# Kernel optimization log

Measured on AMD Instinct MI355X. Metric: run time of the kernel, lower is better.

The kernel has to match this reference:

```python
import jax, jax.numpy as jnp
import numpy as np

INPUT_DIM = 128
NUM_CLASSES = 10
MAX_DEPTH = 8
HID = 16            # effective_transform_output_dim
TEMP = 1.0
EFF_IN = INPUT_DIM + 2          # root features + parent score + grandparent score
N_INTERNAL = 2 ** MAX_DEPTH - 1  # 255, level-order stacked
N_LEAVES = 2 ** MAX_DEPTH        # 256
BATCH = 32768


def setup_inputs() -> dict:
    key = jax.random.key(0)
    ks = jax.random.split(key, 6)
    x = jax.random.normal(ks[0], (BATCH, INPUT_DIM), jnp.float32)
    path_prob = jnp.ones((BATCH, 1), jnp.float32)
    W1 = jax.random.normal(ks[1], (N_INTERNAL, EFF_IN, HID), jnp.float32) * (1.0 / np.sqrt(EFF_IN))
    b1 = jax.random.normal(ks[2], (N_INTERNAL, HID), jnp.float32) * 0.01
    w2 = jax.random.normal(ks[3], (N_INTERNAL, HID), jnp.float32) * (1.0 / np.sqrt(HID))
    b2 = jax.random.normal(ks[4], (N_INTERNAL,), jnp.float32) * 0.01
    leaf_logits = jax.random.normal(ks[5], (N_LEAVES, NUM_CLASSES), jnp.float32)
    return {"x": x, "path_prob": path_prob, "W1": W1, "b1": b1,
            "w2": w2, "b2": b2, "leaf_logits": leaf_logits}


def reference(x, path_prob, W1, b1, w2, b2, leaf_logits):
    """Depth-batched soft binary tree: all 2^d nodes at depth d are processed
    as one batched GEMM instead of the original sequential recursion."""
    B = x.shape[0]
    pp = path_prob                              # [B, n_nodes_at_depth]
    parent = jnp.zeros((B, 1), x.dtype)         # parent decision scores (0 => unused at depth 0)
    grandp = jnp.zeros((B, 1), x.dtype)         # grandparent scores (0 => unused at depth 0,1)
    for d in range(MAX_DEPTH):
        lo, hi = 2 ** d - 1, 2 ** (d + 1) - 1   # level-order slice of this depth's nodes
        W1d = W1[lo:hi]                          # [N, EFF_IN, HID]
        # concat([x, parent, grandparent]) @ W1d without materializing the concat
        h = jnp.einsum('be,neh->bnh', x, W1d[:, :INPUT_DIM, :])
        h = h + parent[:, :, None] * W1d[None, :, INPUT_DIM, :]
        h = h + grandp[:, :, None] * W1d[None, :, INPUT_DIM + 1, :]
        t = jax.nn.relu(h + b1[lo:hi][None])                       # [B, N, HID]
        score = jnp.einsum('bnh,nh->bn', t, w2[lo:hi]) + b2[lo:hi][None]  # [B, N]
        p = jax.nn.sigmoid(score / TEMP)
        n = pp.shape[1]
        # children: left gets p, right gets 1-p; level-order interleave
        pp = jnp.stack([pp * p, pp * (1.0 - p)], axis=-1).reshape(B, 2 * n)
        grandp = jnp.repeat(parent, 2, axis=1)   # child's grandparent = node's parent
        parent = jnp.repeat(score, 2, axis=1)    # child's parent_out = this node's raw score
    # leaves: sum_n path_prob[:, n] * output_logits[n]
    return jnp.einsum('bn,nc->bc', pp, leaf_logits)
```

## Files before the change

kernel.cpp:

```cpp
#include <hip/hip_runtime.h>
#include <math.h>

namespace {

typedef __attribute__((ext_vector_type(8))) __fp16 f16x8;
typedef __attribute__((ext_vector_type(4))) float f32x4;

constexpr int IN_DIM = 128;
constexpr int EFF    = 130 * 16;
constexpr int NODES  = 255;
constexpr int TS     = 64;
constexpr int BLOCK  = 256;
constexpr int NC     = 10;

__global__ __launch_bounds__(256) void prep_w1(const float* __restrict__ W1,
                                               f16x8* __restrict__ wfrag) {
    __shared__ float xs[IN_DIM * 16];
    const int n = blockIdx.x, tid = threadIdx.x;
    const float4* src = (const float4*)(W1 + (size_t)n * EFF);
    ((float4*)xs)[tid]       = src[tid];
    ((float4*)xs)[tid + 256] = src[tid + 256];
    __syncthreads();
    const int l = tid & 63, t = tid >> 6;
    const int k0 = t * 32 + (l >> 4) * 8, hid = l & 15;
    f16x8 hv;
    #pragma unroll
    for (int j = 0; j < 8; ++j)
        hv[j] = (__fp16)xs[(k0 + j) * 16 + hid];
    wfrag[(n * 4 + t) * 64 + l] = hv;
}

__global__ __launch_bounds__(BLOCK) __attribute__((amdgpu_waves_per_eu(2, 2)))
void tree_mfma(
    const float* __restrict__ x, const float* __restrict__ path_prob,
    const float* __restrict__ W1, const float* __restrict__ b1,
    const float* __restrict__ w2, const float* __restrict__ b2,
    const float* __restrict__ leaf_logits,
    const f16x8* __restrict__ wfrag,
    float* __restrict__ out)
{
    __shared__ float pp[128][TS];
    __shared__ float scbuf[112][TS];

    const int tid  = threadIdx.x;
    const int wv   = tid >> 6, l = tid & 63;
    const int quad = l >> 4,   col = l & 15;
    const int s0   = blockIdx.x * TS;

    if (tid < TS) pp[0][tid] = path_prob[s0 + tid];

    f16x8 xh[4][4];
    #pragma unroll
    for (int t = 0; t < 4; ++t)
        #pragma unroll
        for (int mt = 0; mt < 4; ++mt) {
            const float* xp = x + (size_t)(s0 + mt * 16 + col) * IN_DIM + t * 32 + quad * 8;
            float4 v0 = ((const float4*)xp)[0];
            float4 v1 = ((const float4*)xp)[1];
            float vv[8] = {v0.x, v0.y, v0.z, v0.w, v1.x, v1.y, v1.z, v1.w};
            f16x8 hv;
            #pragma unroll
            for (int j = 0; j < 8; ++j) hv[j] = (__fp16)vv[j];
            xh[t][mt] = hv;
        }

    const int wbase[3] = {0, 64, 80};

    const int first_n = (wv == 0) ? 0 : (wv == 1) ? 2 : (wv == 2) ? 5 : 6;
    f16x8 wcur[4];
    #pragma unroll
    for (int t = 0; t < 4; ++t) wcur[t] = wfrag[(size_t)first_n * 256 + t * 64 + l];

    for (int d = 0; d < 7; ++d) {
        const int nd = 1 << d;
        float (*scW)[TS]  = (float(*)[TS])&scbuf[wbase[d % 3]][0];
        float (*scP)[TS]  = (float(*)[TS])&scbuf[wbase[(d + 2) % 3]][0];
        float (*scP2)[TS] = (float(*)[TS])&scbuf[wbase[(d + 1) % 3]][0];
        const int stride = 128 >> d, half = 64 >> d;

        for (int nl = wv; nl < nd; nl += 4) {
            const int n = nd - 1 + nl;
            const int nn = (nl + 4 < nd) ? (n + 4) : (2 * nd - 1 + wv);

            f16x8 wnext[4];
            {
                const f16x8* wnp = wfrag + (size_t)nn * 256 + l;
                #pragma unroll
                for (int t = 0; t < 4; ++t) wnext[t] = wnp[t * 64];
            }

            const float4 b1q = ((const float4*)(b1 + n * 16))[quad];
            const float4 w2q = ((const float4*)(w2 + n * 16))[quad];
            const float4 wpq = ((const float4*)(W1 + (size_t)n * EFF + 128 * 16))[quad];
            const float4 wgq = ((const float4*)(W1 + (size_t)n * EFF + 129 * 16))[quad];
            const float  b2v = b2[n];
            const int    slot = nl * stride;
            const float  ppar = pp[slot][l];
            float par[4], gp[4];
            #pragma unroll
            for (int mt = 0; mt < 4; ++mt) {
                const int scol = mt * 16 + col;
                par[mt] = (d >= 1) ? scP[nl >> 1][scol] : 0.0f;
                gp[mt]  = (d >= 2) ? scP2[nl >> 2][scol] : 0.0f;
            }

            f32x4 binit = {b1q.x, b1q.y, b1q.z, b1q.w};
            f32x4 acc[4] = {binit, binit, binit, binit};
            #pragma unroll
            for (int t = 0; t < 4; ++t) {
                #pragma unroll
                for (int mt = 0; mt < 4; ++mt)
                    acc[mt] = __builtin_amdgcn_mfma_f32_16x16x32_f16(wcur[t], xh[t][mt], acc[mt], 0, 0, 0);
            }

            float score01[4];
            #pragma unroll
            for (int mt = 0; mt < 4; ++mt) {
                const f32x4 a = acc[mt];
                const float pa = par[mt], ga = gp[mt];
                float ts = 0.0f;
                #pragma unroll
                for (int r = 0; r < 4; ++r) {
                    const float wpr = (r == 0) ? wpq.x : (r == 1) ? wpq.y : (r == 2) ? wpq.z : wpq.w;
                    const float wgr = (r == 0) ? wgq.x : (r == 1) ? wgq.y : (r == 2) ? wgq.z : wgq.w;
                    const float w2r = (r == 0) ? w2q.x : (r == 1) ? w2q.y : (r == 2) ? w2q.z : w2q.w;
                    const float h = fmaf(pa, wpr, fmaf(ga, wgr, a[r]));
                    ts = fmaf(fmaxf(h, 0.0f), w2r, ts);
                }
                ts += __shfl_xor(ts, 16);
                ts += __shfl_xor(ts, 32);
                score01[mt] = ts;
            }
            const float sa = (quad & 1) ? score01[1] : score01[0];
            const float sb = (quad & 1) ? score01[3] : score01[2];
            const float sv = ((quad & 2) ? sb : sa) + b2v;

            scW[nl][l] = sv;
            const float p = 1.0f / (1.0f + __expf(-sv));
            pp[slot][l]        = ppar * p;
            pp[slot + half][l] = ppar * (1.0f - p);

            #pragma unroll
            for (int t = 0; t < 4; ++t) wcur[t] = wnext[t];
        }
        __syncthreads();
    }

    float oacc[NC];
    #pragma unroll
    for (int c = 0; c < NC; ++c) oacc[c] = 0.0f;
    {
        float (*scP)[TS]  = (float(*)[TS])&scbuf[wbase[0]][0];
        float (*scP2)[TS] = (float(*)[TS])&scbuf[wbase[2]][0];

        for (int nl = wv; nl < 128; nl += 4) {
            const int n = 127 + nl;
            const int nn = (nl + 4 < 128) ? (n + 4) : 254;

            f16x8 wnext[4];
            {
                const f16x8* wnp = wfrag + (size_t)nn * 256 + l;
                #pragma unroll
                for (int t = 0; t < 4; ++t) wnext[t] = wnp[t * 64];
            }

            const float4 b1q = ((const float4*)(b1 + n * 16))[quad];
            const float4 w2q = ((const float4*)(w2 + n * 16))[quad];
            const float4 wpq = ((const float4*)(W1 + (size_t)n * EFF + 128 * 16))[quad];
            const float4 wgq = ((const float4*)(W1 + (size_t)n * EFF + 129 * 16))[quad];
            const float  b2v = b2[n];
            const float  ppar = pp[nl][l];
            float par[4], gp[4];
            #pragma unroll
            for (int mt = 0; mt < 4; ++mt) {
                const int scol = mt * 16 + col;
                par[mt] = scP[nl >> 1][scol];
                gp[mt]  = scP2[nl >> 2][scol];
            }

            f32x4 binit = {b1q.x, b1q.y, b1q.z, b1q.w};
            f32x4 acc[4] = {binit, binit, binit, binit};
            #pragma unroll
            for (int t = 0; t < 4; ++t) {
                #pragma unroll
                for (int mt = 0; mt < 4; ++mt)
                    acc[mt] = __builtin_amdgcn_mfma_f32_16x16x32_f16(wcur[t], xh[t][mt], acc[mt], 0, 0, 0);
            }

            float score01[4];
            #pragma unroll
            for (int mt = 0; mt < 4; ++mt) {
                const f32x4 a = acc[mt];
                const float pa = par[mt], ga = gp[mt];
                float ts = 0.0f;
                #pragma unroll
                for (int r = 0; r < 4; ++r) {
                    const float wpr = (r == 0) ? wpq.x : (r == 1) ? wpq.y : (r == 2) ? wpq.z : wpq.w;
                    const float wgr = (r == 0) ? wgq.x : (r == 1) ? wgq.y : (r == 2) ? wgq.z : wgq.w;
                    const float w2r = (r == 0) ? w2q.x : (r == 1) ? w2q.y : (r == 2) ? w2q.z : w2q.w;
                    const float h = fmaf(pa, wpr, fmaf(ga, wgr, a[r]));
                    ts = fmaf(fmaxf(h, 0.0f), w2r, ts);
                }
                ts += __shfl_xor(ts, 16);
                ts += __shfl_xor(ts, 32);
                score01[mt] = ts;
            }
            const float sa = (quad & 1) ? score01[1] : score01[0];
            const float sb = (quad & 1) ? score01[3] : score01[2];
            const float sv = ((quad & 2) ? sb : sa) + b2v;

            const float p = 1.0f / (1.0f + __expf(-sv));
            const float pL = ppar * p;
            const float pR = ppar * (1.0f - p);
            const float* llp = leaf_logits + (size_t)(2 * nl) * NC;
            #pragma unroll
            for (int c = 0; c < NC; ++c)
                oacc[c] = fmaf(pL, llp[c], fmaf(pR, llp[NC + c], oacc[c]));

            #pragma unroll
            for (int t = 0; t < 4; ++t) wcur[t] = wnext[t];
        }
    }

    __syncthreads();
    {
        float* red = &scbuf[0][0];
        #pragma unroll
        for (int c = 0; c < NC; ++c)
            red[(wv * 64 + l) * NC + c] = oacc[c];
    }
    __syncthreads();
    {
        const float* red = &scbuf[0][0];
        for (int i = tid; i < TS * NC; i += BLOCK) {
            float v = red[i] + red[640 + i] + red[1280 + i] + red[1920 + i];
            out[(size_t)s0 * NC + i] = v;
        }
    }
}

}

extern "C" void kernel_launch(void* const* d_in, const int* in_sizes, int n_in,
                              void* d_out, int out_size, void* d_ws, size_t ws_size,
                              hipStream_t stream) {
    const float* x           = (const float*)d_in[0];
    const float* path_prob   = (const float*)d_in[1];
    const float* W1          = (const float*)d_in[2];
    const float* b1          = (const float*)d_in[3];
    const float* w2          = (const float*)d_in[4];
    const float* b2          = (const float*)d_in[5];
    const float* leaf_logits = (const float*)d_in[6];
    float* out = (float*)d_out;

    const int batch = in_sizes[0] / IN_DIM;
    f16x8* wfrag = (f16x8*)d_ws;

    hipLaunchKernelGGL(prep_w1, dim3(NODES), dim3(256), 0, stream, W1, wfrag);
    hipLaunchKernelGGL(tree_mfma, dim3(batch / TS), dim3(BLOCK), 0, stream,
                       x, path_prob, W1, b1, w2, b2, leaf_logits, wfrag, out);
}
```

Before: 150.5 us.

## Software-pipeline node epilogue behind next node's weight load and MFMA

Replaces the register prefetch of the next node's weight fragments with a software pipeline. Each iteration loads its own weights, then runs the previous node's score epilogue (ReLU, w2 dot, sigmoid, pp/score stores) while that load is in flight, and only then issues its own MFMAs. The idea is to hide global load latency behind VALU work and to overlap the epilogue with MFMA execution. In exchange, the weight load is no longer a full iteration ahead, and more state (accumulators and per-node params) stays live, adding register pressure at two waves per EU.

```diff
diff --git a/kernel.cpp b/kernel.cpp
--- a/kernel.cpp
+++ b/kernel.cpp
@@ -30,6 +30,47 @@
     wfrag[(n * 4 + t) * 64 + l] = hv;
 }
 
+__device__ __forceinline__ void loadW(const f16x8* __restrict__ wfrag, int n, int l,
+                                      f16x8 (&w)[4]) {
+    const f16x8* wp = wfrag + (size_t)n * 256 + l;
+    #pragma unroll
+    for (int t = 0; t < 4; ++t) w[t] = wp[t * 64];
+}
+
+__device__ __forceinline__ void mfma16(const f16x8 (&w)[4], const f16x8 (&xh)[4][4],
+                                       f32x4 (&acc)[4]) {
+    #pragma unroll
+    for (int t = 0; t < 4; ++t)
+        #pragma unroll
+        for (int mt = 0; mt < 4; ++mt)
+            acc[mt] = __builtin_amdgcn_mfma_f32_16x16x32_f16(w[t], xh[t][mt], acc[mt], 0, 0, 0);
+}
+
+__device__ __forceinline__ float epilogue_score(
+    const f32x4 (&acc)[4], const float4& w2q, const float4& wpq, const float4& wgq,
+    const float (&par)[4], const float (&gp)[4], float b2v, int quad)
+{
+    float score01[4];
+    #pragma unroll
+    for (int mt = 0; mt < 4; ++mt) {
+        float ts = 0.0f;
+        #pragma unroll
+        for (int r = 0; r < 4; ++r) {
+            const float wpr = (r == 0) ? wpq.x : (r == 1) ? wpq.y : (r == 2) ? wpq.z : wpq.w;
+            const float wgr = (r == 0) ? wgq.x : (r == 1) ? wgq.y : (r == 2) ? wgq.z : wgq.w;
+            const float w2r = (r == 0) ? w2q.x : (r == 1) ? w2q.y : (r == 2) ? w2q.z : w2q.w;
+            const float h = fmaf(par[mt], wpr, fmaf(gp[mt], wgr, acc[mt][r]));
+            ts = fmaf(fmaxf(h, 0.0f), w2r, ts);
+        }
+        ts += __shfl_xor(ts, 16);
+        ts += __shfl_xor(ts, 32);
+        score01[mt] = ts;
+    }
+    const float sa = (quad & 1) ? score01[1] : score01[0];
+    const float sb = (quad & 1) ? score01[3] : score01[2];
+    return ((quad & 2) ? sb : sa) + b2v;
+}
+
 __global__ __launch_bounds__(BLOCK) __attribute__((amdgpu_waves_per_eu(2, 2)))
 void tree_mfma(
     const float* __restrict__ x, const float* __restrict__ path_prob,
@@ -66,11 +107,6 @@
 
     const int wbase[3] = {0, 64, 80};
 
-    const int first_n = (wv == 0) ? 0 : (wv == 1) ? 2 : (wv == 2) ? 5 : 6;
-    f16x8 wcur[4];
-    #pragma unroll
-    for (int t = 0; t < 4; ++t) wcur[t] = wfrag[(size_t)first_n * 256 + t * 64 + l];
-
     for (int d = 0; d < 7; ++d) {
         const int nd = 1 << d;
         float (*scW)[TS]  = (float(*)[TS])&scbuf[wbase[d % 3]][0];
@@ -78,18 +114,28 @@
         float (*scP2)[TS] = (float(*)[TS])&scbuf[wbase[(d + 1) % 3]][0];
         const int stride = 128 >> d, half = 64 >> d;
 
+        bool havePrev = false;
+        f32x4 accP[4];
+        float4 p_w2q, p_wpq, p_wgq;
+        float  p_b2v = 0.f, p_ppar = 0.f;
+        float  p_par[4], p_gp[4];
+        int    p_slot = 0, p_nl = 0;
+
         for (int nl = wv; nl < nd; nl += 4) {
             const int n = nd - 1 + nl;
-            const int nn = (nl + 4 < nd) ? (n + 4) : (2 * nd - 1 + wv);
-
-            f16x8 wnext[4];
-            {
-                const f16x8* wnp = wfrag + (size_t)nn * 256 + l;
-                #pragma unroll
-                for (int t = 0; t < 4; ++t) wnext[t] = wnp[t * 64];
-            }
-
+
+            f16x8 w[4];
+            loadW(wfrag, n, l, w);
             const float4 b1q = ((const float4*)(b1 + n * 16))[quad];
+
+            if (havePrev) {
+                const float sv = epilogue_score(accP, p_w2q, p_wpq, p_wgq, p_par, p_gp, p_b2v, quad);
+                scW[p_nl][l] = sv;
+                const float p = 1.0f / (1.0f + __expf(-sv));
+                pp[p_slot][l]        = p_ppar * p;
+                pp[p_slot + half][l] = p_ppar * (1.0f - p);
+            }
+
             const float4 w2q = ((const float4*)(w2 + n * 16))[quad];
             const float4 wpq = ((const float4*)(W1 + (size_t)n * EFF + 128 * 16))[quad];
             const float4 wgq = ((const float4*)(W1 + (size_t)n * EFF + 129 * 16))[quad];
@@ -106,42 +152,23 @@
 
             f32x4 binit = {b1q.x, b1q.y, b1q.z, b1q.w};
             f32x4 acc[4] = {binit, binit, binit, binit};
-            #pragma unroll
-            for (int t = 0; t < 4; ++t) {
-                #pragma unroll
-                for (int mt = 0; mt < 4; ++mt)
-                    acc[mt] = __builtin_amdgcn_mfma_f32_16x16x32_f16(wcur[t], xh[t][mt], acc[mt], 0, 0, 0);
-            }
-
-            float score01[4];
-            #pragma unroll
-            for (int mt = 0; mt < 4; ++mt) {
-                const f32x4 a = acc[mt];
-                const float pa = par[mt], ga = gp[mt];
-                float ts = 0.0f;
-                #pragma unroll
-                for (int r = 0; r < 4; ++r) {
-                    const float wpr = (r == 0) ? wpq.x : (r == 1) ? wpq.y : (r == 2) ? wpq.z : wpq.w;
-                    const float wgr = (r == 0) ? wgq.x : (r == 1) ? wgq.y : (r == 2) ? wgq.z : wgq.w;
-                    const float w2r = (r == 0) ? w2q.x : (r == 1) ? w2q.y : (r == 2) ? w2q.z : w2q.w;
-                    const float h = fmaf(pa, wpr, fmaf(ga, wgr, a[r]));
-                    ts = fmaf(fmaxf(h, 0.0f), w2r, ts);
-                }
-                ts += __shfl_xor(ts, 16);
-                ts += __shfl_xor(ts, 32);
-                score01[mt] = ts;
-            }
-            const float sa = (quad & 1) ? score01[1] : score01[0];
-            const float sb = (quad & 1) ? score01[3] : score01[2];
-            const float sv = ((quad & 2) ? sb : sa) + b2v;
-
-            scW[nl][l] = sv;
+            mfma16(w, xh, acc);
+
+            #pragma unroll
+            for (int mt = 0; mt < 4; ++mt) accP[mt] = acc[mt];
+            p_w2q = w2q; p_wpq = wpq; p_wgq = wgq;
+            p_b2v = b2v; p_ppar = ppar;
+            #pragma unroll
+            for (int mt = 0; mt < 4; ++mt) { p_par[mt] = par[mt]; p_gp[mt] = gp[mt]; }
+            p_slot = slot; p_nl = nl;
+            havePrev = true;
+        }
+        if (havePrev) {
+            const float sv = epilogue_score(accP, p_w2q, p_wpq, p_wgq, p_par, p_gp, p_b2v, quad);
+            scW[p_nl][l] = sv;
             const float p = 1.0f / (1.0f + __expf(-sv));
-            pp[slot][l]        = ppar * p;
-            pp[slot + half][l] = ppar * (1.0f - p);
-
-            #pragma unroll
-            for (int t = 0; t < 4; ++t) wcur[t] = wnext[t];
+            pp[p_slot][l]        = p_ppar * p;
+            pp[p_slot + half][l] = p_ppar * (1.0f - p);
         }
         __syncthreads();
     }
@@ -153,18 +180,31 @@
         float (*scP)[TS]  = (float(*)[TS])&scbuf[wbase[0]][0];
         float (*scP2)[TS] = (float(*)[TS])&scbuf[wbase[2]][0];
 
+        bool havePrev = false;
+        f32x4 accP[4];
+        float4 p_w2q, p_wpq, p_wgq;
+        float  p_b2v = 0.f, p_ppar = 0.f;
+        float  p_par[4], p_gp[4];
+        int    p_nl = 0;
+
         for (int nl = wv; nl < 128; nl += 4) {
             const int n = 127 + nl;
-            const int nn = (nl + 4 < 128) ? (n + 4) : 254;
-
-            f16x8 wnext[4];
-            {
-                const f16x8* wnp = wfrag + (size_t)nn * 256 + l;
+
+            f16x8 w[4];
+            loadW(wfrag, n, l, w);
+            const float4 b1q = ((const float4*)(b1 + n * 16))[quad];
+
+            if (havePrev) {
+                const float sv = epilogue_score(accP, p_w2q, p_wpq, p_wgq, p_par, p_gp, p_b2v, quad);
+                const float p = 1.0f / (1.0f + __expf(-sv));
+                const float pL = p_ppar * p;
+                const float pR = p_ppar * (1.0f - p);
+                const float* llp = leaf_logits + (size_t)(2 * p_nl) * NC;
                 #pragma unroll
-                for (int t = 0; t < 4; ++t) wnext[t] = wnp[t * 64];
-            }
-
-            const float4 b1q = ((const float4*)(b1 + n * 16))[quad];
+                for (int c = 0; c < NC; ++c)
+                    oacc[c] = fmaf(pL, llp[c], fmaf(pR, llp[NC + c], oacc[c]));
+            }
+
             const float4 w2q = ((const float4*)(w2 + n * 16))[quad];
             const float4 wpq = ((const float4*)(W1 + (size_t)n * EFF + 128 * 16))[quad];
             const float4 wgq = ((const float4*)(W1 + (size_t)n * EFF + 129 * 16))[quad];
@@ -180,45 +220,26 @@
 
             f32x4 binit = {b1q.x, b1q.y, b1q.z, b1q.w};
             f32x4 acc[4] = {binit, binit, binit, binit};
-            #pragma unroll
-            for (int t = 0; t < 4; ++t) {
-                #pragma unroll
-                for (int mt = 0; mt < 4; ++mt)
-                    acc[mt] = __builtin_amdgcn_mfma_f32_16x16x32_f16(wcur[t], xh[t][mt], acc[mt], 0, 0, 0);
-            }
-
-            float score01[4];
-            #pragma unroll
-            for (int mt = 0; mt < 4; ++mt) {
-                const f32x4 a = acc[mt];
-                const float pa = par[mt], ga = gp[mt];
-                float ts = 0.0f;
-                #pragma unroll
-                for (int r = 0; r < 4; ++r) {
-                    const float wpr = (r == 0) ? wpq.x : (r == 1) ? wpq.y : (r == 2) ? wpq.z : wpq.w;
-                    const float wgr = (r == 0) ? wgq.x : (r == 1) ? wgq.y : (r == 2) ? wgq.z : wgq.w;
-                    const float w2r = (r == 0) ? w2q.x : (r == 1) ? w2q.y : (r == 2) ? w2q.z : w2q.w;
-                    const float h = fmaf(pa, wpr, fmaf(ga, wgr, a[r]));
-                    ts = fmaf(fmaxf(h, 0.0f), w2r, ts);
-                }
-                ts += __shfl_xor(ts, 16);
-                ts += __shfl_xor(ts, 32);
-                score01[mt] = ts;
-            }
-            const float sa = (quad & 1) ? score01[1] : score01[0];
-            const float sb = (quad & 1) ? score01[3] : score01[2];
-            const float sv = ((quad & 2) ? sb : sa) + b2v;
-
+            mfma16(w, xh, acc);
+
+            #pragma unroll
+            for (int mt = 0; mt < 4; ++mt) accP[mt] = acc[mt];
+            p_w2q = w2q; p_wpq = wpq; p_wgq = wgq;
+            p_b2v = b2v; p_ppar = ppar;
+            #pragma unroll
+            for (int mt = 0; mt < 4; ++mt) { p_par[mt] = par[mt]; p_gp[mt] = gp[mt]; }
+            p_nl = nl;
+            havePrev = true;
+        }
+        if (havePrev) {
+            const float sv = epilogue_score(accP, p_w2q, p_wpq, p_wgq, p_par, p_gp, p_b2v, quad);
             const float p = 1.0f / (1.0f + __expf(-sv));
-            const float pL = ppar * p;
-            const float pR = ppar * (1.0f - p);
-            const float* llp = leaf_logits + (size_t)(2 * nl) * NC;
+            const float pL = p_ppar * p;
+            const float pR = p_ppar * (1.0f - p);
+            const float* llp = leaf_logits + (size_t)(2 * p_nl) * NC;
             #pragma unroll
             for (int c = 0; c < NC; ++c)
                 oacc[c] = fmaf(pL, llp[c], fmaf(pR, llp[NC + c], oacc[c]));
-
-            #pragma unroll
-            for (int t = 0; t < 4; ++t) wcur[t] = wnext[t];
         }
     }
 
```

Measured after the change: 140.1 us. 1.07x faster.
